# Optimization experiments

Measured on AMD Instinct MI355X. Metric: run time of the kernel, lower is better.

Reference implementation:

```python
import jax, jax.numpy as jnp
import numpy as np

D_INNER, D_STATE, DT_RANK = 2048, 16, 128
BATCH, SEQ = 2, 2048


def setup_inputs() -> dict:
    key = jax.random.key(0)
    ks = jax.random.split(key, 6)
    x = jax.random.normal(ks[0], (BATCH, SEQ, D_INNER), dtype=jnp.float32)
    # A_log initialized uniform(-4, -1) per _init_parameters
    A_log = jax.random.uniform(ks[1], (D_INNER, D_STATE), minval=-4.0, maxval=-1.0, dtype=jnp.float32)
    D = jnp.ones((D_INNER,), dtype=jnp.float32)
    # torch Linear weights: [out_features, in_features], kaiming-uniform-ish scale
    x_proj_w = jax.random.normal(ks[2], (DT_RANK + 2 * D_STATE, D_INNER), dtype=jnp.float32) / np.sqrt(D_INNER)
    dt_proj_w = jax.random.normal(ks[3], (D_INNER, DT_RANK), dtype=jnp.float32) / np.sqrt(DT_RANK)
    dt_std = DT_RANK ** (-0.5)
    dt_proj_b = jax.random.uniform(ks[4], (D_INNER,), minval=-dt_std, maxval=dt_std, dtype=jnp.float32)
    return {"x": x, "A_log": A_log, "D": D, "x_proj_w": x_proj_w,
            "dt_proj_w": dt_proj_w, "dt_proj_b": dt_proj_b}


def _selective_scan(u, delta, A, B, C, D):
    # u, delta: [b, l, d]; A: [d, n]; B, C: [b, l, n]; D: [d]
    dA = jnp.exp(delta[..., None] * A[None, None])          # [b, l, d, n]
    dBu = (delta * u)[..., None] * B[:, :, None, :]         # [b, l, d, n]

    def step(h, inp):
        dA_t, dBu_t, C_t = inp                              # [b,d,n],[b,d,n],[b,n]
        h = dA_t * h + dBu_t
        y_t = jnp.einsum('bdn,bn->bd', h, C_t)
        return h, y_t

    h0 = jnp.zeros((u.shape[0], u.shape[2], A.shape[1]), dtype=u.dtype)
    xs = (jnp.moveaxis(dA, 1, 0), jnp.moveaxis(dBu, 1, 0), jnp.moveaxis(C, 1, 0))
    _, ys = jax.lax.scan(step, h0, xs)                      # ys: [l, b, d]
    y = jnp.moveaxis(ys, 0, 1)
    return y + u * D[None, None, :]


def reference(x, A_log, D, x_proj_w, dt_proj_w, dt_proj_b):
    # x: [b, l, d_inner]
    x_dbl = jnp.einsum('bld,ed->ble', x, x_proj_w)          # [b, l, dt_rank + 2n]
    delta_r = x_dbl[..., :DT_RANK]
    B = x_dbl[..., DT_RANK:DT_RANK + D_STATE]
    C = x_dbl[..., DT_RANK + D_STATE:]
    delta = jnp.einsum('blr,dr->bld', delta_r, dt_proj_w) + dt_proj_b
    delta = jax.nn.softplus(delta)                          # delta_softplus=True
    A = -jnp.exp(A_log)
    return _selective_scan(x, delta, A, B, C, D)
```

## Files before the change

kernel.cpp:

```cpp
#include <hip/hip_runtime.h>
#include <hip/hip_bf16.h>
#include <math.h>

#define DI   2048
#define DS   16
#define DTR  128
#define NBATCH 2
#define SEQ  2048
#define ROWS (NBATCH*SEQ)
#define NE   (DTR + 2*DS)
#define NC   32
#define LC   (SEQ/NC)
#define KS1  8

typedef float f32x4 __attribute__((ext_vector_type(4)));
typedef short s16x8 __attribute__((ext_vector_type(8)));
typedef short s16x4 __attribute__((ext_vector_type(4)));

__device__ inline short f2bf(float f) {
    unsigned u = __builtin_bit_cast(unsigned, f);
    u += 0x7FFFu + ((u >> 16) & 1u);
    return (short)(u >> 16);
}

__device__ inline unsigned pk2(float lo, float hi) {
    union { __hip_bfloat162 h; unsigned u; } cv;
    cv.h = __float22bfloat162_rn(float2{lo, hi});
    return cv.u;
}

__global__ __launch_bounds__(256) void k_castw(const float* __restrict__ w,
                                               const float* __restrict__ dtw,
                                               short* __restrict__ wb,
                                               short* __restrict__ dtwb) {
    int i = blockIdx.x*256 + threadIdx.x;
    if (i < 81920) {
        float4 v = ((const float4*)w)[i];
        s16x4 o = { f2bf(v.x), f2bf(v.y), f2bf(v.z), f2bf(v.w) };
        *(s16x4*)(wb + 4*i) = o;
    } else if (i < 147456) {
        int j = i - 81920;
        float4 v = ((const float4*)dtw)[j];
        s16x4 o = { f2bf(v.x), f2bf(v.y), f2bf(v.z), f2bf(v.w) };
        *(s16x4*)(dtwb + 4*j) = o;
    }
}

__global__ __launch_bounds__(256) void k_gemm1(const float* __restrict__ x,
                                               const short* __restrict__ wb,
                                               float* __restrict__ part) {
    const int wave = blockIdx.x*4 + (threadIdx.x >> 6);
    const int lane = threadIdx.x & 63;
    const int m16 = wave & 255;
    const int ks  = wave >> 8;
    const int r = lane & 15, g = lane >> 4;
    f32x4 acc[10];
    #pragma unroll
    for (int i = 0; i < 10; i++) acc[i] = (f32x4){0.f,0.f,0.f,0.f};

    const float* xp = x + (size_t)(m16*16 + r)*DI + g*8;
    #pragma unroll 2
    for (int kk = 0; kk < 8; ++kk) {
        const int k0 = ks*256 + kk*32;
        float4 xa = *(const float4*)(xp + k0);
        float4 xc = *(const float4*)(xp + k0 + 4);
        union { s16x8 v; unsigned u[4]; } af;
        af.u[0] = pk2(xa.x, xa.y);
        af.u[1] = pk2(xa.z, xa.w);
        af.u[2] = pk2(xc.x, xc.y);
        af.u[3] = pk2(xc.z, xc.w);
        const short* bp = wb + (size_t)r*DI + k0 + g*8;
        #pragma unroll
        for (int nf = 0; nf < 10; ++nf) {
            s16x8 bfrag = *(const s16x8*)(bp + (size_t)nf*16*DI);
            acc[nf] = __builtin_amdgcn_mfma_f32_16x16x32_bf16(af.v, bfrag, acc[nf], 0, 0, 0);
        }
    }
    const int orow = m16*16 + g*4;
    #pragma unroll
    for (int nf = 0; nf < 10; ++nf)
        #pragma unroll
        for (int j = 0; j < 4; ++j)
            part[((size_t)ks*ROWS + orow + j)*NE + nf*16 + r] = acc[nf][j];
}

__global__ __launch_bounds__(256) void k_split(const float* __restrict__ part,
                                               short* __restrict__ dRb,
                                               float* __restrict__ Bm,
                                               float* __restrict__ Cm) {
    int i = blockIdx.x*256 + threadIdx.x;
    if (i >= ROWS*NE) return;
    float v = 0.f;
    #pragma unroll
    for (int s = 0; s < KS1; ++s) v += part[(size_t)s*ROWS*NE + i];
    int row = i / NE, e = i - row*NE;
    if (e < DTR)            dRb[(size_t)row*DTR + e] = f2bf(v);
    else if (e < DTR + DS)  Bm[(size_t)row*DS + (e - DTR)] = v;
    else                    Cm[(size_t)row*DS + (e - DTR - DS)] = v;
}

__global__ __launch_bounds__(256) void k_gemm2(const short* __restrict__ dRb,
                                               const short* __restrict__ dtwb,
                                               const float* __restrict__ bias,
                                               float* __restrict__ delta) {
    const int wave = blockIdx.x*4 + (threadIdx.x >> 6);
    const int lane = threadIdx.x & 63;
    const int m16 = wave >> 5, nt = wave & 31;
    const int r = lane & 15, g = lane >> 4;

    s16x8 a[4];
    const short* ap = dRb + (size_t)(m16*16 + r)*DTR + g*8;
    #pragma unroll
    for (int ks = 0; ks < 4; ++ks) a[ks] = *(const s16x8*)(ap + ks*32);

    f32x4 acc[4];
    #pragma unroll
    for (int i = 0; i < 4; i++) acc[i] = (f32x4){0.f,0.f,0.f,0.f};

    #pragma unroll
    for (int nf = 0; nf < 4; ++nf) {
        const short* bp = dtwb + (size_t)(nt*64 + nf*16 + r)*DTR + g*8;
        #pragma unroll
        for (int ks = 0; ks < 4; ++ks) {
            s16x8 b = *(const s16x8*)(bp + ks*32);
            acc[nf] = __builtin_amdgcn_mfma_f32_16x16x32_bf16(a[ks], b, acc[nf], 0, 0, 0);
        }
    }
    const int orow = m16*16 + g*4;
    #pragma unroll
    for (int nf = 0; nf < 4; ++nf) {
        const int col = nt*64 + nf*16 + r;
        const float bb = bias[col];
        #pragma unroll
        for (int j = 0; j < 4; ++j) {
            float v = acc[nf][j] + bb;
            delta[(size_t)(orow + j)*DI + col] =
                fmaxf(v, 0.f) + __logf(1.f + __expf(-fabsf(v)));
        }
    }
}

__global__ __launch_bounds__(256) void k_scan1(const float* __restrict__ delta,
                                               const float* __restrict__ x,
                                               const float* __restrict__ Bm,
                                               const float* __restrict__ A_log,
                                               float* __restrict__ aprod,
                                               float* __restrict__ rsum) {
    __shared__ float ld[LC][64];
    __shared__ float lx[LC][64];
    __shared__ float lB[LC][DS];
    const int tid = threadIdx.x;
    const int bb = blockIdx.x & 31;
    const int b  = (blockIdx.x >> 5) & 1;
    const int c  = blockIdx.x >> 6;
    const int d0 = bb*64;
    const int lbase = c*LC;

    {
        const float* dsrc = delta + ((size_t)(b*SEQ + lbase))*DI + d0;
        const float* xsrc = x     + ((size_t)(b*SEQ + lbase))*DI + d0;
        const int row = tid >> 4, col = (tid & 15)*4;
        #pragma unroll
        for (int i = 0; i < 4; i++) {
            *(float4*)&ld[row + 16*i][col] = *(const float4*)(dsrc + (size_t)(row + 16*i)*DI + col);
            *(float4*)&lx[row + 16*i][col] = *(const float4*)(xsrc + (size_t)(row + 16*i)*DI + col);
        }
        const float* bsrc = Bm + ((size_t)(b*SEQ + lbase))*DS;
        *(float4*)&lB[tid >> 2][(tid & 3)*4] = *(const float4*)(bsrc + tid*4);
    }

    const int lane = tid & 63, widx = tid >> 6;
    const int dlow = lane & 15, q = lane >> 4;
    const int dcol = widx*16 + dlow;
    const int d = d0 + dcol;
    const int n0 = 4*q;

    float4 Alg = *(const float4*)(A_log + (size_t)d*DS + n0);
    float An[4] = { -__expf(Alg.x), -__expf(Alg.y), -__expf(Alg.z), -__expf(Alg.w) };
    float ap[4] = {1.f,1.f,1.f,1.f}, r[4] = {0.f,0.f,0.f,0.f};

    __syncthreads();

    #pragma unroll 8
    for (int tt = 0; tt < LC; ++tt) {
        float dlt = ld[tt][dcol];
        float u   = lx[tt][dcol];
        float du  = dlt * u;
        float4 bv = *(const float4*)&lB[tt][n0];
        float bbv[4] = {bv.x, bv.y, bv.z, bv.w};
        #pragma unroll
        for (int j = 0; j < 4; ++j) {
            float da = __expf(dlt * An[j]);
            r[j]  = fmaf(da, r[j], du * bbv[j]);
            ap[j] *= da;
        }
    }
    size_t base = (((size_t)c*NBATCH + b)*DI + d)*DS + n0;
    *(float4*)(aprod + base) = (float4){ap[0], ap[1], ap[2], ap[3]};
    *(float4*)(rsum  + base) = (float4){r[0],  r[1],  r[2],  r[3]};
}

__global__ __launch_bounds__(256) void k_mid(const float* __restrict__ aprod,
                                             const float* __restrict__ rsum,
                                             float* __restrict__ hin) {
    int gid = blockIdx.x*256 + threadIdx.x;
    int n = gid & 15;
    int d = (gid >> 4) & (DI-1);
    int b = gid >> 15;
    float h = 0.f;
    for (int c = 0; c < NC; c++) {
        size_t idx = (((size_t)c*NBATCH + b)*DI + d)*DS + n;
        hin[idx] = h;
        h = fmaf(aprod[idx], h, rsum[idx]);
    }
}

__global__ __launch_bounds__(256) void k_scan2(const float* __restrict__ delta,
                                               const float* __restrict__ x,
                                               const float* __restrict__ Bm,
                                               const float* __restrict__ Cm,
                                               const float* __restrict__ A_log,
                                               const float* __restrict__ Dv,
                                               const float* __restrict__ hin,
                                               float* __restrict__ y) {
    __shared__ float ld[LC][64];
    __shared__ float lx[LC][64];
    __shared__ float lB[LC][DS];
    __shared__ float lC[LC][DS];
    const int tid = threadIdx.x;
    const int bb = blockIdx.x & 31;
    const int b  = (blockIdx.x >> 5) & 1;
    const int c  = blockIdx.x >> 6;
    const int d0 = bb*64;
    const int lbase = c*LC;

    {
        const float* dsrc = delta + ((size_t)(b*SEQ + lbase))*DI + d0;
        const float* xsrc = x     + ((size_t)(b*SEQ + lbase))*DI + d0;
        const int row = tid >> 4, col = (tid & 15)*4;
        #pragma unroll
        for (int i = 0; i < 4; i++) {
            *(float4*)&ld[row + 16*i][col] = *(const float4*)(dsrc + (size_t)(row + 16*i)*DI + col);
            *(float4*)&lx[row + 16*i][col] = *(const float4*)(xsrc + (size_t)(row + 16*i)*DI + col);
        }
        const float* bsrc = Bm + ((size_t)(b*SEQ + lbase))*DS;
        const float* csrc = Cm + ((size_t)(b*SEQ + lbase))*DS;
        *(float4*)&lB[tid >> 2][(tid & 3)*4] = *(const float4*)(bsrc + tid*4);
        *(float4*)&lC[tid >> 2][(tid & 3)*4] = *(const float4*)(csrc + tid*4);
    }

    const int lane = tid & 63, widx = tid >> 6;
    const int dlow = lane & 15, q = lane >> 4;
    const int dcol = widx*16 + dlow;
    const int d = d0 + dcol;
    const int n0 = 4*q;

    float4 Alg = *(const float4*)(A_log + (size_t)d*DS + n0);
    float An[4] = { -__expf(Alg.x), -__expf(Alg.y), -__expf(Alg.z), -__expf(Alg.w) };
    size_t base = (((size_t)c*NBATCH + b)*DI + d)*DS + n0;
    float4 hv = *(const float4*)(hin + base);
    float h[4] = {hv.x, hv.y, hv.z, hv.w};
    const float Dd = Dv[d];
    float* yp = y + ((size_t)(b*SEQ + lbase))*DI + d;

    __syncthreads();

    #pragma unroll 8
    for (int tt = 0; tt < LC; ++tt) {
        float dlt = ld[tt][dcol];
        float u   = lx[tt][dcol];
        float du  = dlt * u;
        float4 bv = *(const float4*)&lB[tt][n0];
        float4 cv = *(const float4*)&lC[tt][n0];
        float bbv[4] = {bv.x, bv.y, bv.z, bv.w};
        float ccv[4] = {cv.x, cv.y, cv.z, cv.w};
        float acc = 0.f;
        #pragma unroll
        for (int j = 0; j < 4; ++j) {
            float da = __expf(dlt * An[j]);
            h[j] = fmaf(da, h[j], du * bbv[j]);
            acc  = fmaf(h[j], ccv[j], acc);
        }
        acc += __shfl_xor(acc, 16);
        acc += __shfl_xor(acc, 32);
        if (q == 0) yp[(size_t)tt*DI] = fmaf(u, Dd, acc);
    }
}

extern "C" void kernel_launch(void* const* d_in, const int* in_sizes, int n_in,
                              void* d_out, int out_size, void* d_ws, size_t ws_size,
                              hipStream_t stream) {
    const float* x     = (const float*)d_in[0];
    const float* A_log = (const float*)d_in[1];
    const float* Dv    = (const float*)d_in[2];
    const float* xpw   = (const float*)d_in[3];
    const float* dtw   = (const float*)d_in[4];
    const float* dtb   = (const float*)d_in[5];
    float* out = (float*)d_out;

    const size_t SCN = (size_t)NC*NBATCH*DS*DI;

    float* ws    = (float*)d_ws;
    float* delta = ws;
    float* unionR= delta + (size_t)ROWS*DI;
    float* part  = unionR;
    float* aprod = unionR;
    float* rsum  = aprod + SCN;
    float* hin   = rsum  + SCN;
    float* uend  = unionR + ((3*SCN > (size_t)KS1*ROWS*NE) ? 3*SCN : (size_t)KS1*ROWS*NE);
    float* Bm    = uend;
    float* Cm    = Bm + (size_t)ROWS*DS;
    short* dRb   = (short*)(Cm + (size_t)ROWS*DS);
    short* wb    = dRb + (size_t)ROWS*DTR;
    short* dtwb  = wb  + (size_t)160*2048;

    k_castw<<<576, 256, 0, stream>>>(xpw, dtw, wb, dtwb);
    k_gemm1<<<512, 256, 0, stream>>>(x, wb, part);
    k_split<<<(ROWS*NE + 255)/256, 256, 0, stream>>>(part, dRb, Bm, Cm);
    k_gemm2<<<2048, 256, 0, stream>>>(dRb, dtwb, dtb, delta);
    k_scan1<<<2048, 256, 0, stream>>>(delta, x, Bm, A_log, aprod, rsum);
    k_mid<<<256, 256, 0, stream>>>(aprod, rsum, hin);
    k_scan2<<<2048, 256, 0, stream>>>(delta, x, Bm, Cm, A_log, Dv, hin, out);
}
```

Baseline: 211.8 us.

## Store delta as bf16 and pack with bf16 x in scan LDS; double split-K

The softplus output delta is written as bf16 instead of fp32. The scan kernels load it and pack it with a bf16-rounded x into one 32-bit LDS word, which cuts global and LDS traffic for the scans. The gemm1 split-K factor doubles to 16 with twice the blocks, raising parallelism but doubling the partial-sum buffer that k_split reduces. Rounding both delta and x to bf16 lowers output accuracy, including the u*D skip term.

After: 214.0 us. No clear change (+1.0%).

```diff
diff --git a/kernel.cpp b/kernel.cpp
--- a/kernel.cpp
+++ b/kernel.cpp
@@ -11,7 +11,7 @@
 #define NE   (DTR + 2*DS)
 #define NC   32
 #define LC   (SEQ/NC)
-#define KS1  8
+#define KS1  16
 
 typedef float f32x4 __attribute__((ext_vector_type(4)));
 typedef short s16x8 __attribute__((ext_vector_type(8)));
@@ -27,6 +27,9 @@
     union { __hip_bfloat162 h; unsigned u; } cv;
     cv.h = __float22bfloat162_rn(float2{lo, hi});
     return cv.u;
+}
+__device__ inline unsigned packdu(short dbf, float xf) {
+    return ((unsigned)(unsigned short)f2bf(xf) << 16) | (unsigned)(unsigned short)dbf;
 }
 
 __global__ __launch_bounds__(256) void k_castw(const float* __restrict__ w,
@@ -59,9 +62,9 @@
     for (int i = 0; i < 10; i++) acc[i] = (f32x4){0.f,0.f,0.f,0.f};
 
     const float* xp = x + (size_t)(m16*16 + r)*DI + g*8;
-    #pragma unroll 2
-    for (int kk = 0; kk < 8; ++kk) {
-        const int k0 = ks*256 + kk*32;
+    #pragma unroll
+    for (int kk = 0; kk < 4; ++kk) {
+        const int k0 = ks*128 + kk*32;
         float4 xa = *(const float4*)(xp + k0);
         float4 xc = *(const float4*)(xp + k0 + 4);
         union { s16x8 v; unsigned u[4]; } af;
@@ -102,7 +105,7 @@
 __global__ __launch_bounds__(256) void k_gemm2(const short* __restrict__ dRb,
                                                const short* __restrict__ dtwb,
                                                const float* __restrict__ bias,
-                                               float* __restrict__ delta) {
+                                               unsigned short* __restrict__ deltab) {
     const int wave = blockIdx.x*4 + (threadIdx.x >> 6);
     const int lane = threadIdx.x & 63;
     const int m16 = wave >> 5, nt = wave & 31;
@@ -134,20 +137,19 @@
         #pragma unroll
         for (int j = 0; j < 4; ++j) {
             float v = acc[nf][j] + bb;
-            delta[(size_t)(orow + j)*DI + col] =
-                fmaxf(v, 0.f) + __logf(1.f + __expf(-fabsf(v)));
-        }
-    }
-}
-
-__global__ __launch_bounds__(256) void k_scan1(const float* __restrict__ delta,
+            float sp = fmaxf(v, 0.f) + __logf(1.f + __expf(-fabsf(v)));
+            deltab[(size_t)(orow + j)*DI + col] = (unsigned short)f2bf(sp);
+        }
+    }
+}
+
+__global__ __launch_bounds__(256) void k_scan1(const unsigned short* __restrict__ deltab,
                                                const float* __restrict__ x,
                                                const float* __restrict__ Bm,
                                                const float* __restrict__ A_log,
                                                float* __restrict__ aprod,
                                                float* __restrict__ rsum) {
-    __shared__ float ld[LC][64];
-    __shared__ float lx[LC][64];
+    __shared__ unsigned lxd[LC][64];
     __shared__ float lB[LC][DS];
     const int tid = threadIdx.x;
     const int bb = blockIdx.x & 31;
@@ -157,13 +159,19 @@
     const int lbase = c*LC;
 
     {
-        const float* dsrc = delta + ((size_t)(b*SEQ + lbase))*DI + d0;
-        const float* xsrc = x     + ((size_t)(b*SEQ + lbase))*DI + d0;
+        const unsigned short* dsrc = deltab + ((size_t)(b*SEQ + lbase))*DI + d0;
+        const float*          xsrc = x      + ((size_t)(b*SEQ + lbase))*DI + d0;
         const int row = tid >> 4, col = (tid & 15)*4;
         #pragma unroll
         for (int i = 0; i < 4; i++) {
-            *(float4*)&ld[row + 16*i][col] = *(const float4*)(dsrc + (size_t)(row + 16*i)*DI + col);
-            *(float4*)&lx[row + 16*i][col] = *(const float4*)(xsrc + (size_t)(row + 16*i)*DI + col);
+            s16x4  dv = *(const s16x4*) (dsrc + (size_t)(row + 16*i)*DI + col);
+            float4 xv = *(const float4*)(xsrc + (size_t)(row + 16*i)*DI + col);
+            uint4 o;
+            o.x = packdu(dv[0], xv.x);
+            o.y = packdu(dv[1], xv.y);
+            o.z = packdu(dv[2], xv.z);
+            o.w = packdu(dv[3], xv.w);
+            *(uint4*)&lxd[row + 16*i][col] = o;
         }
         const float* bsrc = Bm + ((size_t)(b*SEQ + lbase))*DS;
         *(float4*)&lB[tid >> 2][(tid & 3)*4] = *(const float4*)(bsrc + tid*4);
@@ -183,8 +191,9 @@
 
     #pragma unroll 8
     for (int tt = 0; tt < LC; ++tt) {
-        float dlt = ld[tt][dcol];
-        float u   = lx[tt][dcol];
+        unsigned v = lxd[tt][dcol];
+        float dlt = __builtin_bit_cast(float, v << 16);
+        float u   = __builtin_bit_cast(float, v & 0xffff0000u);
         float du  = dlt * u;
         float4 bv = *(const float4*)&lB[tt][n0];
         float bbv[4] = {bv.x, bv.y, bv.z, bv.w};
@@ -215,7 +224,7 @@
     }
 }
 
-__global__ __launch_bounds__(256) void k_scan2(const float* __restrict__ delta,
+__global__ __launch_bounds__(256) void k_scan2(const unsigned short* __restrict__ deltab,
                                                const float* __restrict__ x,
                                                const float* __restrict__ Bm,
                                                const float* __restrict__ Cm,
@@ -223,8 +232,7 @@
                                                const float* __restrict__ Dv,
                                                const float* __restrict__ hin,
                                                float* __restrict__ y) {
-    __shared__ float ld[LC][64];
-    __shared__ float lx[LC][64];
+    __shared__ unsigned lxd[LC][64];
     __shared__ float lB[LC][DS];
     __shared__ float lC[LC][DS];
     const int tid = threadIdx.x;
@@ -235,13 +243,19 @@
     const int lbase = c*LC;
 
     {
-        const float* dsrc = delta + ((size_t)(b*SEQ + lbase))*DI + d0;
-        const float* xsrc = x     + ((size_t)(b*SEQ + lbase))*DI + d0;
+        const unsigned short* dsrc = deltab + ((size_t)(b*SEQ + lbase))*DI + d0;
+        const float*          xsrc = x      + ((size_t)(b*SEQ + lbase))*DI + d0;
         const int row = tid >> 4, col = (tid & 15)*4;
         #pragma unroll
         for (int i = 0; i < 4; i++) {
-            *(float4*)&ld[row + 16*i][col] = *(const float4*)(dsrc + (size_t)(row + 16*i)*DI + col);
-            *(float4*)&lx[row + 16*i][col] = *(const float4*)(xsrc + (size_t)(row + 16*i)*DI + col);
+            s16x4  dv = *(const s16x4*) (dsrc + (size_t)(row + 16*i)*DI + col);
+            float4 xv = *(const float4*)(xsrc + (size_t)(row + 16*i)*DI + col);
+            uint4 o;
+            o.x = packdu(dv[0], xv.x);
+            o.y = packdu(dv[1], xv.y);
+            o.z = packdu(dv[2], xv.z);
+            o.w = packdu(dv[3], xv.w);
+            *(uint4*)&lxd[row + 16*i][col] = o;
         }
         const float* bsrc = Bm + ((size_t)(b*SEQ + lbase))*DS;
         const float* csrc = Cm + ((size_t)(b*SEQ + lbase))*DS;
@@ -267,8 +281,9 @@
 
     #pragma unroll 8
     for (int tt = 0; tt < LC; ++tt) {
-        float dlt = ld[tt][dcol];
-        float u   = lx[tt][dcol];
+        unsigned v = lxd[tt][dcol];
+        float dlt = __builtin_bit_cast(float, v << 16);
+        float u   = __builtin_bit_cast(float, v & 0xffff0000u);
         float du  = dlt * u;
         float4 bv = *(const float4*)&lB[tt][n0];
         float4 cv = *(const float4*)&lC[tt][n0];
@@ -299,15 +314,16 @@
     float* out = (float*)d_out;
 
     const size_t SCN = (size_t)NC*NBATCH*DS*DI;
+    const size_t PARTN = (size_t)KS1*ROWS*NE;
 
     float* ws    = (float*)d_ws;
-    float* delta = ws;
-    float* unionR= delta + (size_t)ROWS*DI;
+    unsigned short* deltab = (unsigned short*)ws;
+    float* unionR= ws + ((size_t)ROWS*DI/2);
     float* part  = unionR;
     float* aprod = unionR;
     float* rsum  = aprod + SCN;
     float* hin   = rsum  + SCN;
-    float* uend  = unionR + ((3*SCN > (size_t)KS1*ROWS*NE) ? 3*SCN : (size_t)KS1*ROWS*NE);
+    float* uend  = unionR + ((3*SCN > PARTN) ? 3*SCN : PARTN);
     float* Bm    = uend;
     float* Cm    = Bm + (size_t)ROWS*DS;
     short* dRb   = (short*)(Cm + (size_t)ROWS*DS);
@@ -315,10 +331,10 @@
     short* dtwb  = wb  + (size_t)160*2048;
 
     k_castw<<<576, 256, 0, stream>>>(xpw, dtw, wb, dtwb);
-    k_gemm1<<<512, 256, 0, stream>>>(x, wb, part);
+    k_gemm1<<<1024, 256, 0, stream>>>(x, wb, part);
     k_split<<<(ROWS*NE + 255)/256, 256, 0, stream>>>(part, dRb, Bm, Cm);
-    k_gemm2<<<2048, 256, 0, stream>>>(dRb, dtwb, dtb, delta);
-    k_scan1<<<2048, 256, 0, stream>>>(delta, x, Bm, A_log, aprod, rsum);
+    k_gemm2<<<2048, 256, 0, stream>>>(dRb, dtwb, dtb, deltab);
+    k_scan1<<<2048, 256, 0, stream>>>(deltab, x, Bm, A_log, aprod, rsum);
     k_mid<<<256, 256, 0, stream>>>(aprod, rsum, hin);
-    k_scan2<<<2048, 256, 0, stream>>>(delta, x, Bm, Cm, A_log, Dv, hin, out);
-}
+    k_scan2<<<2048, 256, 0, stream>>>(deltab, x, Bm, Cm, A_log, Dv, hin, out);
+}
```
